# Kernel optimization log

Measured on AMD Instinct MI355X. Metric: run time of the kernel, lower is better.

## Reference

```python
import jax, jax.numpy as jnp
import numpy as np

B, L, D_MODEL, EXPAND, HEADDIM, QK_DIM = 2, 512, 512, 2, 128, 16
D_INNER = EXPAND * D_MODEL            # 1024
NHEADS = D_INNER // HEADDIM           # 8
EPS = 1e-3
STD_DEV = 1.0 / np.sqrt(2 * L * QK_DIM)
TWO_PI = 2.0 * np.pi


def setup_inputs() -> dict:
    key = jax.random.key(0)
    kv, kq, kk = jax.random.split(key, 3)
    v = jax.random.normal(kv, (B, L, D_INNER), dtype=jnp.float32)
    q = jax.random.normal(kq, (B, L, NHEADS * QK_DIM), dtype=jnp.float32)
    k = jax.random.normal(kk, (B, L, NHEADS * QK_DIM), dtype=jnp.float32)
    return {"v": v, "q": q, "k": k}


def reference(v, q, k):
    b, l, dim = v.shape
    residual = v
    # b l (n h) -> b l n h
    vh = v.reshape(b, l, NHEADS, HEADDIM)
    # b l (n d) -> b n d l
    qh = q.reshape(b, l, NHEADS, QK_DIM).transpose(0, 2, 3, 1)
    kh = k.reshape(b, l, NHEADS, QK_DIM).transpose(0, 2, 3, 1)
    pos = jnp.arange(l, dtype=v.dtype)  # position indices
    c = jnp.asarray(TWO_PI * EPS, dtype=v.dtype)
    # q_matrix[b,n,d,t,l] = cos(c * q[b,n,d,t] * pos[l])
    q_mat = jnp.cos(c * qh[:, :, :, :, None] * pos)
    # k_matrix[b,n,d,l,t] = cos(c * k[b,n,d,t] * pos[l])
    k_mat = jnp.cos(c * kh[:, :, :, None, :] * pos[:, None])
    sym = (q_mat - k_mat).sum(axis=2)  # (b, n, t, l)
    out = jnp.einsum('bntl,blnh->btnh', sym, vh)
    out = jnp.asarray(STD_DEV, v.dtype) * out
    return out.reshape(b, l, dim) + residual
```

## Files before the change

### kernel.cpp

```cpp
#include <hip/hip_runtime.h>

#define L_SEQ   512
#define NHEADS_ 8
#define HEADDIM_ 128
#define QKD     16
#define DINNER  1024
#define EPS_F   1e-3f
#define STD_F   0.0078125f

#define KS_ROW  529

typedef __attribute__((ext_vector_type(8))) short  short8;
typedef __attribute__((ext_vector_type(4))) float  floatx4;
typedef __attribute__((ext_vector_type(2))) float  float2v;

__device__ __forceinline__ float cosrev(float rev) {
    float r = rev - floorf(rev);
    return __builtin_amdgcn_cosf(r);
}

__device__ __forceinline__ float two_cos_small(float a) {
    float x = a * a;
    return fmaf(fmaf(x, 129.8787876f, -39.4784176f), x, 2.0f);
}

__device__ __forceinline__ unsigned short f2bf_rne(float x) {
    union { float f; unsigned int u; } v;
    v.f = x;
    unsigned int r = v.u + 0x7fffu + ((v.u >> 16) & 1u);
    return (unsigned short)(r >> 16);
}
__device__ __forceinline__ unsigned short f2bf_fast(float x) {
    union { float f; unsigned int u; } v;
    v.f = x;
    return (unsigned short)((v.u + 0x8000u) >> 16);
}

__global__ __launch_bounds__(256) void vtrans_kernel(const float* __restrict__ v,
                                                     unsigned short* __restrict__ vt) {
    const int bid = blockIdx.x;
    const int tid = threadIdx.x;
    const int l0 = (bid & 7) * 64;
    const int h0 = ((bid >> 3) & 1) * 64;
    const int bn = bid >> 4;
    const int b = bn >> 3, n = bn & 7;
    __shared__ float tile[64][65];
    const float* vb = v + ((size_t)b * L_SEQ) * DINNER + n * HEADDIM_;
#pragma unroll
    for (int i = 0; i < 16; ++i) {
        int f = i * 256 + tid;
        int hh = f & 63, ll = f >> 6;
        tile[hh][ll] = vb[(size_t)(l0 + ll) * DINNER + (h0 + hh)];
    }
    __syncthreads();
    unsigned short* vdst = vt + (size_t)bn * (64 * 128 * 8);
#pragma unroll
    for (int i = 0; i < 2; ++i) {
        int f = i * 256 + tid;
        int hh = f & 63;
        int lc = f >> 6;
        short8 pk;
#pragma unroll
        for (int j = 0; j < 8; ++j)
            pk[j] = (short)f2bf_rne(tile[hh][lc * 8 + j]);
        *(short8*)(vdst + ((size_t)((l0 >> 3) + lc) * 128 + (h0 + hh)) * 8) = pk;
    }
}

__global__ __launch_bounds__(256, 3) void vand_fused(const float* __restrict__ v,
                                                     const float* __restrict__ q,
                                                     const float* __restrict__ k,
                                                     const unsigned short* __restrict__ vt,
                                                     float* __restrict__ out) {
    const int tid  = threadIdx.x;
    const int w    = tid >> 6;
    const int lane = tid & 63;
    const int tl   = lane & 15;
    const int quad = lane >> 4;
    const int ttile = blockIdx.x;
    const int bn    = blockIdx.y;
    const int b = bn >> 3, n = bn & 7;
    const float t0f = (float)(ttile * 16);

    __shared__ float smem[16 * KS_ROW];
    float* ksl = smem;

#pragma unroll
    for (int rep = 0; rep < 2; ++rep) {
        const int l = w * 128 + rep * 64 + lane;
        const float* krow = k + ((size_t)(b * L_SEQ + l)) * (NHEADS_ * QKD) + n * QKD;
        float kk[16];
#pragma unroll
        for (int d4 = 0; d4 < 4; ++d4) {
            float4 t4 = *(const float4*)(krow + 4 * d4);
            kk[d4 * 4 + 0] = t4.x; kk[d4 * 4 + 1] = t4.y;
            kk[d4 * 4 + 2] = t4.z; kk[d4 * 4 + 3] = t4.w;
        }
        float2v M2[8], C1[8], C0[8];
#pragma unroll
        for (int i = 0; i < 8; ++i) {
            float a0 = EPS_F * kk[2 * i], a1 = EPS_F * kk[2 * i + 1];
            M2[i].x = two_cos_small(a0);         M2[i].y = two_cos_small(a1);
            C1[i].x = cosrev(a0 * t0f);          C1[i].y = cosrev(a1 * t0f);
            C0[i].x = cosrev(a0 * (t0f - 1.f));  C0[i].y = cosrev(a1 * (t0f - 1.f));
        }
        const int base = (l >> 5) * 33 + (l & 31);
#pragma unroll
        for (int m = 0; m < 16; ++m) {
            float2v s = ((C1[0] + C1[1]) + (C1[2] + C1[3]))
                      + ((C1[4] + C1[5]) + (C1[6] + C1[7]));
            ksl[m * KS_ROW + base] = s.x + s.y;
#pragma unroll
            for (int i = 0; i < 8; ++i) {
                float2v nx = M2[i] * C1[i] - C0[i];
                C0[i] = C1[i];
                C1[i] = nx;
            }
        }
    }

    const int   t   = ttile * 16 + tl;
    const int   l0  = w * 128 + quad * 32;
    const float l0f = (float)l0;

    const float* qrow = q + ((size_t)(b * L_SEQ + t)) * (NHEADS_ * QKD) + n * QKD;
    float2v M2[8], C1[8], C0[8];
#pragma unroll
    for (int d4 = 0; d4 < 4; ++d4) {
        float4 qq = *(const float4*)(qrow + 4 * d4);
        float aa[4] = {EPS_F * qq.x, EPS_F * qq.y, EPS_F * qq.z, EPS_F * qq.w};
#pragma unroll
        for (int e = 0; e < 2; ++e) {
            int i = d4 * 2 + e;
            float a0 = aa[2 * e], a1 = aa[2 * e + 1];
            M2[i].x = two_cos_small(a0);         M2[i].y = two_cos_small(a1);
            C1[i].x = cosrev(a0 * l0f);          C1[i].y = cosrev(a1 * l0f);
            C0[i].x = cosrev(a0 * (l0f - 1.f));  C0[i].y = cosrev(a1 * (l0f - 1.f));
        }
    }

    const unsigned short* vrow = vt + (size_t)bn * (64 * 128 * 8);
    const int vbaseoff = (w * 16 + quad * 4) * 1024 + tl * 8;
    const int klds = tl * KS_ROW + (4 * w + quad) * 33;

    floatx4 acc[8] = {};

#pragma unroll
    for (int c = 0; c < 4; ++c) {
        float kv[8];
#pragma unroll
        for (int jj = 0; jj < 8; ++jj) kv[jj] = ksl[klds + c * 8 + jj];
        short8 af;
#pragma unroll
        for (int jj = 0; jj < 8; ++jj) {
            float2v sv = ((C1[0] + C1[1]) + (C1[2] + C1[3]))
                       + ((C1[4] + C1[5]) + (C1[6] + C1[7]));
            float s = (sv.x + sv.y) - kv[jj];
            af[jj] = (short)f2bf_fast(s);
#pragma unroll
            for (int i = 0; i < 8; ++i) {
                float2v nx = M2[i] * C1[i] - C0[i];
                C0[i] = C1[i];
                C1[i] = nx;
            }
        }
#pragma unroll
        for (int ht = 0; ht < 8; ++ht) {
            const short8 bfr = *(const short8*)((const short*)vrow +
                                  vbaseoff + c * 1024 + ht * 128);
            acc[ht] = __builtin_amdgcn_mfma_f32_16x16x32_bf16(af, bfr, acc[ht], 0, 0, 0);
        }
    }

    __syncthreads();
    float (*red)[64][33] = (float (*)[64][33])smem;
#pragma unroll
    for (int ht = 0; ht < 8; ++ht)
#pragma unroll
        for (int r = 0; r < 4; ++r)
            red[w][lane][ht * 4 + r] = acc[ht][r];
    __syncthreads();

    const float* vbase = v   + ((size_t)b * L_SEQ) * DINNER + n * HEADDIM_;
    float*       obase = out + ((size_t)b * L_SEQ) * DINNER + n * HEADDIM_;
#pragma unroll
    for (int i = 0; i < 2; ++i) {
        int g    = i * 256 + tid;
        int hb   = g & 31;
        int tloc = g >> 5;
        int lidx0 = ((tloc >> 2) << 4) + ((hb & 3) << 2);
        int aidx  = ((hb >> 2) << 2) + (tloc & 3);
        float4 sum;
        float* sp = &sum.x;
#pragma unroll
        for (int e = 0; e < 4; ++e) {
            int lidx = lidx0 + e;
            sp[e] = (red[0][lidx][aidx] + red[1][lidx][aidx])
                  + (red[2][lidx][aidx] + red[3][lidx][aidx]);
        }
        size_t gi = (size_t)(ttile * 16 + tloc) * DINNER + hb * 4;
        float4 vres = *(const float4*)(vbase + gi);
        float4 o;
        o.x = fmaf(STD_F, sum.x, vres.x);
        o.y = fmaf(STD_F, sum.y, vres.y);
        o.z = fmaf(STD_F, sum.z, vres.z);
        o.w = fmaf(STD_F, sum.w, vres.w);
        *(float4*)(obase + gi) = o;
    }
}

extern "C" void kernel_launch(void* const* d_in, const int* in_sizes, int n_in,
                              void* d_out, int out_size, void* d_ws, size_t ws_size,
                              hipStream_t stream) {
    const float* v = (const float*)d_in[0];
    const float* q = (const float*)d_in[1];
    const float* k = (const float*)d_in[2];
    float* out = (float*)d_out;
    unsigned short* vt = (unsigned short*)d_ws;

    vtrans_kernel<<<dim3(256), 256, 0, stream>>>(v, vt);
    vand_fused<<<dim3(L_SEQ / 16, 16), 256, 0, stream>>>(v, q, k, vt, out);
}
```

Baseline: 74.61 us.

## Fuse V transpose/bf16 conversion into main kernel, drop pre-pass launch

Removes the separate V transpose-and-convert kernel and instead loads fp32 V directly from global memory inside the MFMA loop, packing it to bf16 with the hardware v_cvt_pk_bf16_f32 instruction. This eliminates one kernel launch and the workspace round trip. The trade-off is that every block now does strided scalar fp32 loads of V (each row 4KB apart) and repeats the conversion, and the 32 t-tiles re-read the same V slice. The A-operand conversion also switches from the truncating-add rounding to the hardware pack instruction.

Measured after the change: 89.87 us. +20.4%, slower.

```diff
diff --git a/kernel.cpp b/kernel.cpp
--- a/kernel.cpp
+++ b/kernel.cpp
@@ -24,53 +24,18 @@
     return fmaf(fmaf(x, 129.8787876f, -39.4784176f), x, 2.0f);
 }
 
-__device__ __forceinline__ unsigned short f2bf_rne(float x) {
-    union { float f; unsigned int u; } v;
-    v.f = x;
-    unsigned int r = v.u + 0x7fffu + ((v.u >> 16) & 1u);
-    return (unsigned short)(r >> 16);
-}
-__device__ __forceinline__ unsigned short f2bf_fast(float x) {
-    union { float f; unsigned int u; } v;
-    v.f = x;
-    return (unsigned short)((v.u + 0x8000u) >> 16);
-}
-
-__global__ __launch_bounds__(256) void vtrans_kernel(const float* __restrict__ v,
-                                                     unsigned short* __restrict__ vt) {
-    const int bid = blockIdx.x;
-    const int tid = threadIdx.x;
-    const int l0 = (bid & 7) * 64;
-    const int h0 = ((bid >> 3) & 1) * 64;
-    const int bn = bid >> 4;
-    const int b = bn >> 3, n = bn & 7;
-    __shared__ float tile[64][65];
-    const float* vb = v + ((size_t)b * L_SEQ) * DINNER + n * HEADDIM_;
+__device__ __forceinline__ short8 pack_bf16x8(const float* s) {
+    union { int i[4]; short8 v; } u;
 #pragma unroll
-    for (int i = 0; i < 16; ++i) {
-        int f = i * 256 + tid;
-        int hh = f & 63, ll = f >> 6;
-        tile[hh][ll] = vb[(size_t)(l0 + ll) * DINNER + (h0 + hh)];
-    }
-    __syncthreads();
-    unsigned short* vdst = vt + (size_t)bn * (64 * 128 * 8);
-#pragma unroll
-    for (int i = 0; i < 2; ++i) {
-        int f = i * 256 + tid;
-        int hh = f & 63;
-        int lc = f >> 6;
-        short8 pk;
-#pragma unroll
-        for (int j = 0; j < 8; ++j)
-            pk[j] = (short)f2bf_rne(tile[hh][lc * 8 + j]);
-        *(short8*)(vdst + ((size_t)((l0 >> 3) + lc) * 128 + (h0 + hh)) * 8) = pk;
-    }
+    for (int p = 0; p < 4; ++p)
+        asm("v_cvt_pk_bf16_f32 %0, %1, %2"
+            : "=v"(u.i[p]) : "v"(s[2 * p]), "v"(s[2 * p + 1]));
+    return u.v;
 }
 
 __global__ __launch_bounds__(256, 3) void vand_fused(const float* __restrict__ v,
                                                      const float* __restrict__ q,
                                                      const float* __restrict__ k,
-                                                     const unsigned short* __restrict__ vt,
                                                      float* __restrict__ out) {
     const int tid  = threadIdx.x;
     const int w    = tid >> 6;
@@ -139,8 +104,7 @@
         }
     }
 
-    const unsigned short* vrow = vt + (size_t)bn * (64 * 128 * 8);
-    const int vbaseoff = (w * 16 + quad * 4) * 1024 + tl * 8;
+    const float* vslice = v + ((size_t)b * L_SEQ) * DINNER + n * HEADDIM_;
     const int klds = tl * KS_ROW + (4 * w + quad) * 33;
 
     floatx4 acc[8] = {};
@@ -150,13 +114,12 @@
         float kv[8];
 #pragma unroll
         for (int jj = 0; jj < 8; ++jj) kv[jj] = ksl[klds + c * 8 + jj];
-        short8 af;
+        float ss[8];
 #pragma unroll
         for (int jj = 0; jj < 8; ++jj) {
             float2v sv = ((C1[0] + C1[1]) + (C1[2] + C1[3]))
                        + ((C1[4] + C1[5]) + (C1[6] + C1[7]));
-            float s = (sv.x + sv.y) - kv[jj];
-            af[jj] = (short)f2bf_fast(s);
+            ss[jj] = (sv.x + sv.y) - kv[jj];
 #pragma unroll
             for (int i = 0; i < 8; ++i) {
                 float2v nx = M2[i] * C1[i] - C0[i];
@@ -164,10 +127,16 @@
                 C1[i] = nx;
             }
         }
+        const short8 af = pack_bf16x8(ss);
+
+        const float* vcp = vslice + (size_t)(w * 128 + quad * 32 + c * 8) * DINNER + tl;
 #pragma unroll
         for (int ht = 0; ht < 8; ++ht) {
-            const short8 bfr = *(const short8*)((const short*)vrow +
-                                  vbaseoff + c * 1024 + ht * 128);
+            float fv[8];
+#pragma unroll
+            for (int jj = 0; jj < 8; ++jj)
+                fv[jj] = vcp[(size_t)jj * DINNER + ht * 16];
+            const short8 bfr = pack_bf16x8(fv);
             acc[ht] = __builtin_amdgcn_mfma_f32_16x16x32_bf16(af, bfr, acc[ht], 0, 0, 0);
         }
     }
@@ -181,8 +150,7 @@
             red[w][lane][ht * 4 + r] = acc[ht][r];
     __syncthreads();
 
-    const float* vbase = v   + ((size_t)b * L_SEQ) * DINNER + n * HEADDIM_;
-    float*       obase = out + ((size_t)b * L_SEQ) * DINNER + n * HEADDIM_;
+    float* obase = out + ((size_t)b * L_SEQ) * DINNER + n * HEADDIM_;
 #pragma unroll
     for (int i = 0; i < 2; ++i) {
         int g    = i * 256 + tid;
@@ -199,7 +167,7 @@
                   + (red[2][lidx][aidx] + red[3][lidx][aidx]);
         }
         size_t gi = (size_t)(ttile * 16 + tloc) * DINNER + hb * 4;
-        float4 vres = *(const float4*)(vbase + gi);
+        float4 vres = *(const float4*)(vslice + gi);
         float4 o;
         o.x = fmaf(STD_F, sum.x, vres.x);
         o.y = fmaf(STD_F, sum.y, vres.y);
@@ -216,8 +184,7 @@
     const float* q = (const float*)d_in[1];
     const float* k = (const float*)d_in[2];
     float* out = (float*)d_out;
-    unsigned short* vt = (unsigned short*)d_ws;
+    (void)d_ws; (void)ws_size;
 
-    vtrans_kernel<<<dim3(256), 256, 0, stream>>>(v, vt);
-    vand_fused<<<dim3(L_SEQ / 16, 16), 256, 0, stream>>>(v, q, k, vt, out);
+    vand_fused<<<dim3(L_SEQ / 16, 16), 256, 0, stream>>>(v, q, k, out);
 }
```

## Double block to 512 threads, halve per-wave l range, prefetch V fragments

Applied to the files above, without the earlier changes.

The fused kernel now launches 512 threads per block, so each of 8 waves covers 64 l positions instead of 128. That halves the serial cosine-recurrence and MFMA chain per wave. V fragments for each chunk are loaded before the recurrence so load latency overlaps the arithmetic. bf16 packing uses the hardware v_cvt_pk_bf16_f32 instruction instead of manual rounding. The cross-wave reduction becomes a two-phase LDS store-then-add, which adds a barrier and more waves competing for registers under the new launch bounds.

After: 74.87 us. Within noise of the previous version (+0.3%).

```diff
diff --git a/kernel.cpp b/kernel.cpp
--- a/kernel.cpp
+++ b/kernel.cpp
@@ -30,10 +30,14 @@
     unsigned int r = v.u + 0x7fffu + ((v.u >> 16) & 1u);
     return (unsigned short)(r >> 16);
 }
-__device__ __forceinline__ unsigned short f2bf_fast(float x) {
-    union { float f; unsigned int u; } v;
-    v.f = x;
-    return (unsigned short)((v.u + 0x8000u) >> 16);
+
+__device__ __forceinline__ short8 pack_bf16x8(const float* s) {
+    union { int i[4]; short8 v; } u;
+#pragma unroll
+    for (int p = 0; p < 4; ++p)
+        asm("v_cvt_pk_bf16_f32 %0, %1, %2"
+            : "=v"(u.i[p]) : "v"(s[2 * p]), "v"(s[2 * p + 1]));
+    return u.v;
 }
 
 __global__ __launch_bounds__(256) void vtrans_kernel(const float* __restrict__ v,
@@ -67,7 +71,7 @@
     }
 }
 
-__global__ __launch_bounds__(256, 3) void vand_fused(const float* __restrict__ v,
+__global__ __launch_bounds__(512, 4) void vand_fused(const float* __restrict__ v,
                                                      const float* __restrict__ q,
                                                      const float* __restrict__ k,
                                                      const unsigned short* __restrict__ vt,
@@ -85,9 +89,8 @@
     __shared__ float smem[16 * KS_ROW];
     float* ksl = smem;
 
-#pragma unroll
-    for (int rep = 0; rep < 2; ++rep) {
-        const int l = w * 128 + rep * 64 + lane;
+    {
+        const int l = w * 64 + lane;
         const float* krow = k + ((size_t)(b * L_SEQ + l)) * (NHEADS_ * QKD) + n * QKD;
         float kk[16];
 #pragma unroll
@@ -120,7 +123,7 @@
     }
 
     const int   t   = ttile * 16 + tl;
-    const int   l0  = w * 128 + quad * 32;
+    const int   l0  = w * 64 + quad * 16;
     const float l0f = (float)l0;
 
     const float* qrow = q + ((size_t)(b * L_SEQ + t)) * (NHEADS_ * QKD) + n * QKD;
@@ -140,23 +143,27 @@
     }
 
     const unsigned short* vrow = vt + (size_t)bn * (64 * 128 * 8);
-    const int vbaseoff = (w * 16 + quad * 4) * 1024 + tl * 8;
-    const int klds = tl * KS_ROW + (4 * w + quad) * 33;
+    const int klds = tl * KS_ROW + (w * 2 + (quad >> 1)) * 33 + (quad & 1) * 16;
 
     floatx4 acc[8] = {};
 
 #pragma unroll
-    for (int c = 0; c < 4; ++c) {
+    for (int c = 0; c < 2; ++c) {
+        short8 bfr[8];
+        const int lcb = (w * 8 + quad * 2 + c) * 128;
+#pragma unroll
+        for (int ht = 0; ht < 8; ++ht)
+            bfr[ht] = *(const short8*)(vrow + (size_t)(lcb + ht * 16 + tl) * 8);
+
         float kv[8];
 #pragma unroll
         for (int jj = 0; jj < 8; ++jj) kv[jj] = ksl[klds + c * 8 + jj];
-        short8 af;
+        float ss[8];
 #pragma unroll
         for (int jj = 0; jj < 8; ++jj) {
             float2v sv = ((C1[0] + C1[1]) + (C1[2] + C1[3]))
                        + ((C1[4] + C1[5]) + (C1[6] + C1[7]));
-            float s = (sv.x + sv.y) - kv[jj];
-            af[jj] = (short)f2bf_fast(s);
+            ss[jj] = (sv.x + sv.y) - kv[jj];
 #pragma unroll
             for (int i = 0; i < 8; ++i) {
                 float2v nx = M2[i] * C1[i] - C0[i];
@@ -164,28 +171,35 @@
                 C1[i] = nx;
             }
         }
-#pragma unroll
-        for (int ht = 0; ht < 8; ++ht) {
-            const short8 bfr = *(const short8*)((const short*)vrow +
-                                  vbaseoff + c * 1024 + ht * 128);
-            acc[ht] = __builtin_amdgcn_mfma_f32_16x16x32_bf16(af, bfr, acc[ht], 0, 0, 0);
-        }
+        const short8 af = pack_bf16x8(ss);
+#pragma unroll
+        for (int ht = 0; ht < 8; ++ht)
+            acc[ht] = __builtin_amdgcn_mfma_f32_16x16x32_bf16(af, bfr[ht], acc[ht], 0, 0, 0);
     }
 
     __syncthreads();
     float (*red)[64][33] = (float (*)[64][33])smem;
-#pragma unroll
-    for (int ht = 0; ht < 8; ++ht)
-#pragma unroll
-        for (int r = 0; r < 4; ++r)
-            red[w][lane][ht * 4 + r] = acc[ht][r];
+    if (w >= 4) {
+#pragma unroll
+        for (int ht = 0; ht < 8; ++ht)
+#pragma unroll
+            for (int r = 0; r < 4; ++r)
+                red[w - 4][lane][ht * 4 + r] = acc[ht][r];
+    }
+    __syncthreads();
+    if (w < 4) {
+#pragma unroll
+        for (int ht = 0; ht < 8; ++ht)
+#pragma unroll
+            for (int r = 0; r < 4; ++r)
+                red[w][lane][ht * 4 + r] += acc[ht][r];
+    }
     __syncthreads();
 
     const float* vbase = v   + ((size_t)b * L_SEQ) * DINNER + n * HEADDIM_;
     float*       obase = out + ((size_t)b * L_SEQ) * DINNER + n * HEADDIM_;
-#pragma unroll
-    for (int i = 0; i < 2; ++i) {
-        int g    = i * 256 + tid;
+    {
+        int g    = tid;
         int hb   = g & 31;
         int tloc = g >> 5;
         int lidx0 = ((tloc >> 2) << 4) + ((hb & 3) << 2);
@@ -219,5 +233,5 @@
     unsigned short* vt = (unsigned short*)d_ws;
 
     vtrans_kernel<<<dim3(256), 256, 0, stream>>>(v, vt);
-    vand_fused<<<dim3(L_SEQ / 16, 16), 256, 0, stream>>>(v, q, k, vt, out);
-}
+    vand_fused<<<dim3(L_SEQ / 16, 16), 512, 0, stream>>>(v, q, k, vt, out);
+}
```

## Prefetch all global loads early, double-buffer V fragments, use hardware bf16 pack

Applied to the files above, without the earlier changes.

Issues the k, q and residual-v global loads at kernel start so their latency overlaps the cosine recurrence. The bf16 V fragments for the next chunk are double-buffered in registers ahead of the MFMAs. The bit-trick bf16 conversion is replaced with the v_cvt_pk_bf16_f32 instruction. The transpose kernel now uses float4 loads, and launch bounds drop from 3 to 2 waves per EU to make room for the extra registers. The cost is higher register pressure and lower occupancy.

Measured after the change: 73.80 us. No clear change (-1.1%).

```diff
diff --git a/kernel.cpp b/kernel.cpp
--- a/kernel.cpp
+++ b/kernel.cpp
@@ -30,10 +30,14 @@
     unsigned int r = v.u + 0x7fffu + ((v.u >> 16) & 1u);
     return (unsigned short)(r >> 16);
 }
-__device__ __forceinline__ unsigned short f2bf_fast(float x) {
-    union { float f; unsigned int u; } v;
-    v.f = x;
-    return (unsigned short)((v.u + 0x8000u) >> 16);
+
+__device__ __forceinline__ short8 pack_bf16x8(const float* s) {
+    union { int i[4]; short8 v; } u;
+#pragma unroll
+    for (int p = 0; p < 4; ++p)
+        asm("v_cvt_pk_bf16_f32 %0, %1, %2"
+            : "=v"(u.i[p]) : "v"(s[2 * p]), "v"(s[2 * p + 1]));
+    return u.v;
 }
 
 __global__ __launch_bounds__(256) void vtrans_kernel(const float* __restrict__ v,
@@ -46,11 +50,21 @@
     const int b = bn >> 3, n = bn & 7;
     __shared__ float tile[64][65];
     const float* vb = v + ((size_t)b * L_SEQ) * DINNER + n * HEADDIM_;
-#pragma unroll
-    for (int i = 0; i < 16; ++i) {
+    float4 r[4];
+#pragma unroll
+    for (int i = 0; i < 4; ++i) {
         int f = i * 256 + tid;
-        int hh = f & 63, ll = f >> 6;
-        tile[hh][ll] = vb[(size_t)(l0 + ll) * DINNER + (h0 + hh)];
+        int hq = f & 15, ll = f >> 4;
+        r[i] = *(const float4*)(vb + (size_t)(l0 + ll) * DINNER + (h0 + hq * 4));
+    }
+#pragma unroll
+    for (int i = 0; i < 4; ++i) {
+        int f = i * 256 + tid;
+        int hq = f & 15, ll = f >> 4;
+        tile[hq * 4 + 0][ll] = r[i].x;
+        tile[hq * 4 + 1][ll] = r[i].y;
+        tile[hq * 4 + 2][ll] = r[i].z;
+        tile[hq * 4 + 3][ll] = r[i].w;
     }
     __syncthreads();
     unsigned short* vdst = vt + (size_t)bn * (64 * 128 * 8);
@@ -67,7 +81,7 @@
     }
 }
 
-__global__ __launch_bounds__(256, 3) void vand_fused(const float* __restrict__ v,
+__global__ __launch_bounds__(256, 2) void vand_fused(const float* __restrict__ v,
                                                      const float* __restrict__ q,
                                                      const float* __restrict__ k,
                                                      const unsigned short* __restrict__ vt,
@@ -85,16 +99,41 @@
     __shared__ float smem[16 * KS_ROW];
     float* ksl = smem;
 
+    float4 kf[2][4];
 #pragma unroll
     for (int rep = 0; rep < 2; ++rep) {
         const int l = w * 128 + rep * 64 + lane;
         const float* krow = k + ((size_t)(b * L_SEQ + l)) * (NHEADS_ * QKD) + n * QKD;
+#pragma unroll
+        for (int d4 = 0; d4 < 4; ++d4)
+            kf[rep][d4] = *(const float4*)(krow + 4 * d4);
+    }
+    const int t = ttile * 16 + tl;
+    const float* qrow = q + ((size_t)(b * L_SEQ + t)) * (NHEADS_ * QKD) + n * QKD;
+    float4 qf[4];
+#pragma unroll
+    for (int d4 = 0; d4 < 4; ++d4)
+        qf[d4] = *(const float4*)(qrow + 4 * d4);
+    const float* vbase = v + ((size_t)b * L_SEQ) * DINNER + n * HEADDIM_;
+    float4 vres[2];
+    size_t gis[2];
+#pragma unroll
+    for (int i = 0; i < 2; ++i) {
+        int g    = i * 256 + tid;
+        int hb   = g & 31;
+        int tloc = g >> 5;
+        gis[i] = (size_t)(ttile * 16 + tloc) * DINNER + hb * 4;
+        vres[i] = *(const float4*)(vbase + gis[i]);
+    }
+
+#pragma unroll
+    for (int rep = 0; rep < 2; ++rep) {
+        const int l = w * 128 + rep * 64 + lane;
         float kk[16];
 #pragma unroll
         for (int d4 = 0; d4 < 4; ++d4) {
-            float4 t4 = *(const float4*)(krow + 4 * d4);
-            kk[d4 * 4 + 0] = t4.x; kk[d4 * 4 + 1] = t4.y;
-            kk[d4 * 4 + 2] = t4.z; kk[d4 * 4 + 3] = t4.w;
+            kk[d4 * 4 + 0] = kf[rep][d4].x; kk[d4 * 4 + 1] = kf[rep][d4].y;
+            kk[d4 * 4 + 2] = kf[rep][d4].z; kk[d4 * 4 + 3] = kf[rep][d4].w;
         }
         float2v M2[8], C1[8], C0[8];
 #pragma unroll
@@ -119,16 +158,20 @@
         }
     }
 
-    const int   t   = ttile * 16 + tl;
+    const unsigned short* vrow = vt + (size_t)bn * (64 * 128 * 8);
+    const int vbaseoff = (w * 16 + quad * 4) * 1024 + tl * 8;
+    short8 bfr[2][8];
+#pragma unroll
+    for (int ht = 0; ht < 8; ++ht)
+        bfr[0][ht] = *(const short8*)((const short*)vrow + vbaseoff + ht * 128);
+
     const int   l0  = w * 128 + quad * 32;
     const float l0f = (float)l0;
-
-    const float* qrow = q + ((size_t)(b * L_SEQ + t)) * (NHEADS_ * QKD) + n * QKD;
     float2v M2[8], C1[8], C0[8];
 #pragma unroll
     for (int d4 = 0; d4 < 4; ++d4) {
-        float4 qq = *(const float4*)(qrow + 4 * d4);
-        float aa[4] = {EPS_F * qq.x, EPS_F * qq.y, EPS_F * qq.z, EPS_F * qq.w};
+        float aa[4] = {EPS_F * qf[d4].x, EPS_F * qf[d4].y,
+                       EPS_F * qf[d4].z, EPS_F * qf[d4].w};
 #pragma unroll
         for (int e = 0; e < 2; ++e) {
             int i = d4 * 2 + e;
@@ -139,24 +182,26 @@
         }
     }
 
-    const unsigned short* vrow = vt + (size_t)bn * (64 * 128 * 8);
-    const int vbaseoff = (w * 16 + quad * 4) * 1024 + tl * 8;
     const int klds = tl * KS_ROW + (4 * w + quad) * 33;
-
     floatx4 acc[8] = {};
 
 #pragma unroll
     for (int c = 0; c < 4; ++c) {
+        if (c < 3) {
+#pragma unroll
+            for (int ht = 0; ht < 8; ++ht)
+                bfr[(c + 1) & 1][ht] = *(const short8*)((const short*)vrow +
+                                          vbaseoff + (c + 1) * 1024 + ht * 128);
+        }
         float kv[8];
 #pragma unroll
         for (int jj = 0; jj < 8; ++jj) kv[jj] = ksl[klds + c * 8 + jj];
-        short8 af;
+        float ss[8];
 #pragma unroll
         for (int jj = 0; jj < 8; ++jj) {
             float2v sv = ((C1[0] + C1[1]) + (C1[2] + C1[3]))
                        + ((C1[4] + C1[5]) + (C1[6] + C1[7]));
-            float s = (sv.x + sv.y) - kv[jj];
-            af[jj] = (short)f2bf_fast(s);
+            ss[jj] = (sv.x + sv.y) - kv[jj];
 #pragma unroll
             for (int i = 0; i < 8; ++i) {
                 float2v nx = M2[i] * C1[i] - C0[i];
@@ -164,12 +209,11 @@
                 C1[i] = nx;
             }
         }
-#pragma unroll
-        for (int ht = 0; ht < 8; ++ht) {
-            const short8 bfr = *(const short8*)((const short*)vrow +
-                                  vbaseoff + c * 1024 + ht * 128);
-            acc[ht] = __builtin_amdgcn_mfma_f32_16x16x32_bf16(af, bfr, acc[ht], 0, 0, 0);
-        }
+        const short8 af = pack_bf16x8(ss);
+#pragma unroll
+        for (int ht = 0; ht < 8; ++ht)
+            acc[ht] = __builtin_amdgcn_mfma_f32_16x16x32_bf16(af, bfr[c & 1][ht],
+                                                              acc[ht], 0, 0, 0);
     }
 
     __syncthreads();
@@ -181,8 +225,7 @@
             red[w][lane][ht * 4 + r] = acc[ht][r];
     __syncthreads();
 
-    const float* vbase = v   + ((size_t)b * L_SEQ) * DINNER + n * HEADDIM_;
-    float*       obase = out + ((size_t)b * L_SEQ) * DINNER + n * HEADDIM_;
+    float* obase = out + ((size_t)b * L_SEQ) * DINNER + n * HEADDIM_;
 #pragma unroll
     for (int i = 0; i < 2; ++i) {
         int g    = i * 256 + tid;
@@ -198,14 +241,12 @@
             sp[e] = (red[0][lidx][aidx] + red[1][lidx][aidx])
                   + (red[2][lidx][aidx] + red[3][lidx][aidx]);
         }
-        size_t gi = (size_t)(ttile * 16 + tloc) * DINNER + hb * 4;
-        float4 vres = *(const float4*)(vbase + gi);
         float4 o;
-        o.x = fmaf(STD_F, sum.x, vres.x);
-        o.y = fmaf(STD_F, sum.y, vres.y);
-        o.z = fmaf(STD_F, sum.z, vres.z);
-        o.w = fmaf(STD_F, sum.w, vres.w);
-        *(float4*)(obase + gi) = o;
+        o.x = fmaf(STD_F, sum.x, vres[i].x);
+        o.y = fmaf(STD_F, sum.y, vres[i].y);
+        o.z = fmaf(STD_F, sum.z, vres[i].z);
+        o.w = fmaf(STD_F, sum.w, vres[i].w);
+        *(float4*)(obase + gis[i]) = o;
     }
 }
 
```
